# Performance work log

Measured on AMD Instinct MI355X. Metric: run time of the kernel, lower is better.

Reference implementation:

```python
import jax, jax.numpy as jnp
import numpy as np

IMG_CENTER = 112.0  # init arg; normalize() is unused in forward
EPS = 1e-12


def setup_inputs() -> dict:
    key = jax.random.key(0)
    kp, kg, km = jax.random.split(key, 3)
    B, N, M = 8, 4096, 4096
    pred = jax.random.normal(kp, (B, N, 3), jnp.float32)
    gt = jax.random.normal(kg, (B, M, 3), jnp.float32)
    # near-identity extrinsics with z-translation 5 so the perspective divide is stable
    base = jnp.concatenate([jnp.eye(3, dtype=jnp.float32),
                            jnp.array([[0.0], [0.0], [5.0]], jnp.float32)], axis=1)  # [3,4]
    proMatrix = base[None, :, :] + 0.05 * jax.random.normal(km, (B, 3, 4), jnp.float32)
    return {"pred": pred, "gt": gt, "proMatrix": proMatrix}


def _project(x, P):
    # x: [B, n, 3], P: [B, 3, 4] -> [B, n, 2] image-plane coords
    B, n, _ = x.shape
    hom = jnp.concatenate([x, jnp.ones((B, n, 1), x.dtype)], axis=2)  # [B, n, 4]
    posed = jnp.einsum('bij,bnj->bni', P, hom)                         # [B, n, 3]
    return posed[..., :2] / posed[..., 2:3]


def _chamfer(a, b):
    # a: [B, N, 2], b: [B, M, 2]; L2-norm (not squared) bidirectional chamfer
    d2 = (jnp.sum(a * a, -1)[:, :, None]
          + jnp.sum(b * b, -1)[:, None, :]
          - 2.0 * jnp.einsum('bnd,bmd->bnm', a, b))  # [B, N, M]
    d = jnp.sqrt(jnp.maximum(d2, EPS))
    per_b = jnp.mean(jnp.min(d, axis=2), axis=1) + jnp.mean(jnp.min(d, axis=1), axis=1)
    return jnp.mean(per_b)


def reference(pred, gt, proMatrix):
    gt_plane = _project(gt, proMatrix)
    pred_plane = _project(pred, proMatrix)
    return _chamfer(gt_plane, pred_plane)
```

## Files before the change

kernel.cpp:

```cpp
#include <hip/hip_runtime.h>
#include <math.h>

#define NPTS 4096
#define NB 8
#define TOTAL (2*NB*NPTS)
#define EPSF 1e-12f

__device__ __forceinline__ unsigned fkey(float x){
    unsigned b = __float_as_uint(x);
    return b ^ (unsigned)(((int)b >> 31) | (int)0x80000000);
}
__device__ __forceinline__ float fdecode(unsigned k){
    unsigned b = (k & 0x80000000u) ? (k ^ 0x80000000u) : ~k;
    return __uint_as_float(b);
}

__global__ void project_kernel(const float* __restrict__ pred,
                               const float* __restrict__ gt,
                               const float* __restrict__ P,
                               float4* __restrict__ proj,
                               unsigned* __restrict__ minbuf){
    int i = blockIdx.x * 256 + threadIdx.x;
    minbuf[i] = 0xFFFFFFFFu;
    int set = i >> 15;
    int b   = (i >> 12) & 7;
    int n   = i & 4095;
    const float* src = set ? pred : gt;
    const float* p3  = src + (size_t)(b * NPTS + n) * 3;
    float x = p3[0], y = p3[1], z = p3[2];
    const float* Pb = P + b * 12;
    float px = Pb[0]*x + Pb[1]*y + Pb[2]*z  + Pb[3];
    float py = Pb[4]*x + Pb[5]*y + Pb[6]*z  + Pb[7];
    float pz = Pb[8]*x + Pb[9]*y + Pb[10]*z + Pb[11];
    float ix = px / pz;
    float iy = py / pz;
    proj[i] = make_float4(ix, iy, ix*ix + iy*iy, 0.0f);
}

#define QPT 8
#define CCH 256
__global__ void chamfer_kernel(const float4* __restrict__ proj,
                               unsigned* __restrict__ minbuf){
    __shared__ float4 cand[CCH];
    int bid   = blockIdx.x;
    int chunk = bid & 15;
    int qhalf = (bid >> 4) & 1;
    int b     = (bid >> 5) & 7;
    int dir   = (bid >> 8) & 1;
    int t = threadIdx.x;

    int qbase = dir * (NB*NPTS) + b * NPTS + qhalf * (QPT*256);
    int cbase = (1 - dir) * (NB*NPTS) + b * NPTS + chunk * CCH;

    float4 c = proj[cbase + t];
    cand[t] = make_float4(-2.0f*c.x, -2.0f*c.y, c.z, 0.0f);
    __syncthreads();

    float ax[QPT], ay[QPT], mn[QPT];
    #pragma unroll
    for (int q = 0; q < QPT; ++q){
        float4 a = proj[qbase + t + q*256];
        ax[q] = a.x; ay[q] = a.y; mn[q] = 3.4e38f;
    }

    #pragma unroll 4
    for (int ci = 0; ci < CCH; ++ci){
        float4 cd = cand[ci];
        #pragma unroll
        for (int q = 0; q < QPT; ++q){
            float tt = fmaf(ax[q], cd.x, cd.z);
            tt = fmaf(ay[q], cd.y, tt);
            mn[q] = fminf(mn[q], tt);
        }
    }

    #pragma unroll
    for (int q = 0; q < QPT; ++q){
        atomicMin(minbuf + qbase + t + q*256, fkey(mn[q]));
    }
}

__global__ void reduce1(const float4* __restrict__ proj,
                        const unsigned* __restrict__ minbuf,
                        float* __restrict__ partials){
    __shared__ float sm[256];
    int t = threadIdx.x;
    float s = 0.0f;
    for (int i = blockIdx.x * 256 + t; i < TOTAL; i += gridDim.x * 256){
        float d2 = fdecode(minbuf[i]) + proj[i].z;
        s += sqrtf(fmaxf(d2, EPSF));
    }
    sm[t] = s; __syncthreads();
    #pragma unroll
    for (int o = 128; o > 0; o >>= 1){
        if (t < o) sm[t] += sm[t + o];
        __syncthreads();
    }
    if (t == 0) partials[blockIdx.x] = sm[0];
}

__global__ void reduce2(const float* __restrict__ partials,
                        float* __restrict__ out){
    __shared__ float sm[256];
    int t = threadIdx.x;
    sm[t] = partials[t];
    __syncthreads();
    #pragma unroll
    for (int o = 128; o > 0; o >>= 1){
        if (t < o) sm[t] += sm[t + o];
        __syncthreads();
    }
    if (t == 0) out[0] = sm[0] * (1.0f / 32768.0f);
}

extern "C" void kernel_launch(void* const* d_in, const int* in_sizes, int n_in,
                              void* d_out, int out_size, void* d_ws, size_t ws_size,
                              hipStream_t stream) {
    const float* pred = (const float*)d_in[0];
    const float* gt   = (const float*)d_in[1];
    const float* P    = (const float*)d_in[2];
    float* out = (float*)d_out;

    float4*   proj     = (float4*)d_ws;
    unsigned* minbuf   = (unsigned*)((char*)d_ws + (size_t)TOTAL*16);
    float*    partials = (float*)((char*)d_ws + (size_t)TOTAL*16 + (size_t)TOTAL*4);

    project_kernel<<<TOTAL/256, 256, 0, stream>>>(pred, gt, P, proj, minbuf);
    chamfer_kernel<<<512, 256, 0, stream>>>(proj, minbuf);
    reduce1<<<256, 256, 0, stream>>>(proj, minbuf, partials);
    reduce2<<<1, 256, 0, stream>>>(partials, out);
}
```

Baseline: 34.19 us.

## Fuse projection into chamfer kernel, use packed FMA and per-chunk min buffers

Removes the separate projection kernel: each chamfer block projects its own query and candidate points from the raw inputs, recomputing projections redundantly across blocks. The atomicMin with encoded keys is replaced by writing per-chunk partial minima to a 16x buffer that the reduce kernel min-reduces. The inner loop uses v_pk_fma_f32 inline asm and v_min3_f32 to halve the instruction count per candidate pair. This saves one launch and the atomics, at the cost of more global traffic for the partial-minimum buffer and duplicated projection work.

```diff
diff --git a/kernel.cpp b/kernel.cpp
--- a/kernel.cpp
+++ b/kernel.cpp
@@ -3,44 +3,46 @@
 
 #define NPTS 4096
 #define NB 8
-#define TOTAL (2*NB*NPTS)
+#define NQTOT (2*NB*NPTS)
 #define EPSF 1e-12f
+#define NCHUNK 16
+#define CCH 256
+#define QPT 8
 
-__device__ __forceinline__ unsigned fkey(float x){
-    unsigned b = __float_as_uint(x);
-    return b ^ (unsigned)(((int)b >> 31) | (int)0x80000000);
+typedef float f32x2 __attribute__((ext_vector_type(2)));
+
+static __device__ __forceinline__ f32x2 pk_fma_bx(f32x2 a, f32x2 b, f32x2 c){
+    f32x2 d;
+    asm("v_pk_fma_f32 %0, %1, %2, %3 op_sel:[0,0,0] op_sel_hi:[1,0,0]"
+        : "=v"(d) : "v"(a), "v"(b), "v"(c));
+    return d;
 }
-__device__ __forceinline__ float fdecode(unsigned k){
-    unsigned b = (k & 0x80000000u) ? (k ^ 0x80000000u) : ~k;
-    return __uint_as_float(b);
+static __device__ __forceinline__ f32x2 pk_fma_by(f32x2 a, f32x2 b, f32x2 c){
+    f32x2 d;
+    asm("v_pk_fma_f32 %0, %1, %2, %3 op_sel:[0,1,0] op_sel_hi:[1,1,1]"
+        : "=v"(d) : "v"(a), "v"(b), "v"(c));
+    return d;
+}
+static __device__ __forceinline__ float fmin3(float a, float b, float c){
+    float d;
+    asm("v_min3_f32 %0, %1, %2, %3" : "=v"(d) : "v"(a), "v"(b), "v"(c));
+    return d;
 }
 
-__global__ void project_kernel(const float* __restrict__ pred,
-                               const float* __restrict__ gt,
-                               const float* __restrict__ P,
-                               float4* __restrict__ proj,
-                               unsigned* __restrict__ minbuf){
-    int i = blockIdx.x * 256 + threadIdx.x;
-    minbuf[i] = 0xFFFFFFFFu;
-    int set = i >> 15;
-    int b   = (i >> 12) & 7;
-    int n   = i & 4095;
-    const float* src = set ? pred : gt;
-    const float* p3  = src + (size_t)(b * NPTS + n) * 3;
+static __device__ __forceinline__ void project_pt(const float* __restrict__ p3,
+                                                  const float* __restrict__ Pb,
+                                                  float& ix, float& iy){
     float x = p3[0], y = p3[1], z = p3[2];
-    const float* Pb = P + b * 12;
-    float px = Pb[0]*x + Pb[1]*y + Pb[2]*z  + Pb[3];
-    float py = Pb[4]*x + Pb[5]*y + Pb[6]*z  + Pb[7];
-    float pz = Pb[8]*x + Pb[9]*y + Pb[10]*z + Pb[11];
-    float ix = px / pz;
-    float iy = py / pz;
-    proj[i] = make_float4(ix, iy, ix*ix + iy*iy, 0.0f);
+    float px = fmaf(Pb[0],x, fmaf(Pb[1],y, fmaf(Pb[2],z,  Pb[3])));
+    float py = fmaf(Pb[4],x, fmaf(Pb[5],y, fmaf(Pb[6],z,  Pb[7])));
+    float pz = fmaf(Pb[8],x, fmaf(Pb[9],y, fmaf(Pb[10],z, Pb[11])));
+    ix = px / pz;
+    iy = py / pz;
 }
 
-#define QPT 8
-#define CCH 256
-__global__ void chamfer_kernel(const float4* __restrict__ proj,
-                               unsigned* __restrict__ minbuf){
+__global__ __launch_bounds__(256) void chamfer_fused(
+        const float* __restrict__ pred, const float* __restrict__ gt,
+        const float* __restrict__ P, float* __restrict__ minpart){
     __shared__ float4 cand[CCH];
     int bid   = blockIdx.x;
     int chunk = bid & 15;
@@ -49,47 +51,66 @@
     int dir   = (bid >> 8) & 1;
     int t = threadIdx.x;
 
-    int qbase = dir * (NB*NPTS) + b * NPTS + qhalf * (QPT*256);
-    int cbase = (1 - dir) * (NB*NPTS) + b * NPTS + chunk * CCH;
+    const float* Pb   = P + b * 12;
+    const float* qsrc = dir ? pred : gt;
+    const float* csrc = dir ? gt : pred;
 
-    float4 c = proj[cbase + t];
-    cand[t] = make_float4(-2.0f*c.x, -2.0f*c.y, c.z, 0.0f);
+    {
+        const float* p3 = csrc + (size_t)(b*NPTS + chunk*CCH + t) * 3;
+        float cx, cy; project_pt(p3, Pb, cx, cy);
+        cand[t] = make_float4(-2.0f*cx, -2.0f*cy, fmaf(cx,cx, cy*cy), 0.0f);
+    }
+
+    f32x2 axp[4], ayp[4];
+    float a2[QPT];
+    #pragma unroll
+    for (int q = 0; q < QPT; ++q){
+        int qi = qhalf*(QPT*256) + q*256 + t;
+        const float* p3 = qsrc + (size_t)(b*NPTS + qi) * 3;
+        float ix, iy; project_pt(p3, Pb, ix, iy);
+        axp[q>>1][q&1] = ix;
+        ayp[q>>1][q&1] = iy;
+        a2[q] = fmaf(ix,ix, iy*iy);
+    }
+    float mn[QPT];
+    #pragma unroll
+    for (int q = 0; q < QPT; ++q) mn[q] = 3.4e38f;
+
     __syncthreads();
 
-    float ax[QPT], ay[QPT], mn[QPT];
-    #pragma unroll
-    for (int q = 0; q < QPT; ++q){
-        float4 a = proj[qbase + t + q*256];
-        ax[q] = a.x; ay[q] = a.y; mn[q] = 3.4e38f;
-    }
-
     #pragma unroll 4
-    for (int ci = 0; ci < CCH; ++ci){
-        float4 cd = cand[ci];
+    for (int ci = 0; ci < CCH; ci += 2){
+        float4 cd0 = cand[ci];
+        float4 cd1 = cand[ci+1];
+        f32x2 c0lo = {cd0.x, cd0.y}, c0hi = {cd0.z, cd0.w};
+        f32x2 c1lo = {cd1.x, cd1.y}, c1hi = {cd1.z, cd1.w};
         #pragma unroll
-        for (int q = 0; q < QPT; ++q){
-            float tt = fmaf(ax[q], cd.x, cd.z);
-            tt = fmaf(ay[q], cd.y, tt);
-            mn[q] = fminf(mn[q], tt);
+        for (int p = 0; p < 4; ++p){
+            f32x2 t0 = pk_fma_bx(axp[p], c0lo, c0hi);
+            t0 = pk_fma_by(ayp[p], c0lo, t0);
+            f32x2 t1 = pk_fma_bx(axp[p], c1lo, c1hi);
+            t1 = pk_fma_by(ayp[p], c1lo, t1);
+            mn[2*p]   = fmin3(t0.x, t1.x, mn[2*p]);
+            mn[2*p+1] = fmin3(t0.y, t1.y, mn[2*p+1]);
         }
     }
 
+    int gq = dir*(NB*NPTS) + b*NPTS + qhalf*(QPT*256) + t;
     #pragma unroll
     for (int q = 0; q < QPT; ++q){
-        atomicMin(minbuf + qbase + t + q*256, fkey(mn[q]));
+        minpart[(size_t)chunk*NQTOT + gq + q*256] = mn[q] + a2[q];
     }
 }
 
-__global__ void reduce1(const float4* __restrict__ proj,
-                        const unsigned* __restrict__ minbuf,
-                        float* __restrict__ partials){
+__global__ __launch_bounds__(256) void reduce_min_sum(
+        const float* __restrict__ minpart, float* __restrict__ partials){
     __shared__ float sm[256];
     int t = threadIdx.x;
-    float s = 0.0f;
-    for (int i = blockIdx.x * 256 + t; i < TOTAL; i += gridDim.x * 256){
-        float d2 = fdecode(minbuf[i]) + proj[i].z;
-        s += sqrtf(fmaxf(d2, EPSF));
-    }
+    int i = blockIdx.x * 256 + t;
+    float m0 = minpart[i];
+    #pragma unroll
+    for (int c = 1; c < NCHUNK; ++c) m0 = fminf(m0, minpart[(size_t)c*NQTOT + i]);
+    float s = sqrtf(fmaxf(m0, EPSF));
     sm[t] = s; __syncthreads();
     #pragma unroll
     for (int o = 128; o > 0; o >>= 1){
@@ -99,8 +120,8 @@
     if (t == 0) partials[blockIdx.x] = sm[0];
 }
 
-__global__ void reduce2(const float* __restrict__ partials,
-                        float* __restrict__ out){
+__global__ void reduce_final(const float* __restrict__ partials,
+                             float* __restrict__ out){
     __shared__ float sm[256];
     int t = threadIdx.x;
     sm[t] = partials[t];
@@ -121,12 +142,10 @@
     const float* P    = (const float*)d_in[2];
     float* out = (float*)d_out;
 
-    float4*   proj     = (float4*)d_ws;
-    unsigned* minbuf   = (unsigned*)((char*)d_ws + (size_t)TOTAL*16);
-    float*    partials = (float*)((char*)d_ws + (size_t)TOTAL*16 + (size_t)TOTAL*4);
+    float* minpart  = (float*)d_ws;
+    float* partials = (float*)((char*)d_ws + (size_t)NCHUNK*NQTOT*4);
 
-    project_kernel<<<TOTAL/256, 256, 0, stream>>>(pred, gt, P, proj, minbuf);
-    chamfer_kernel<<<512, 256, 0, stream>>>(proj, minbuf);
-    reduce1<<<256, 256, 0, stream>>>(proj, minbuf, partials);
-    reduce2<<<1, 256, 0, stream>>>(partials, out);
+    chamfer_fused<<<512, 256, 0, stream>>>(pred, gt, P, minpart);
+    reduce_min_sum<<<256, 256, 0, stream>>>(minpart, partials);
+    reduce_final<<<1, 256, 0, stream>>>(partials, out);
 }
```

Measured after the change: 27.99 us. 1.22x faster.
